# Optimization experiments

Hardware: AMD Instinct MI355X
Metric: run time of the kernel (lower is better)

Reference implementation:

```python
import jax, jax.numpy as jnp
import numpy as np

CAPACITY_FACTOR = 1.25


def setup_inputs() -> dict:
    key = jax.random.key(0)
    k1, k2, k3, k4 = jax.random.split(key, 4)
    B, T, H = 2, 2048, 1024
    E, F = 8, 2048
    x = jax.random.normal(k1, (B, T, H), dtype=jnp.float32)
    Wr = jax.random.normal(k2, (H, E), dtype=jnp.float32) * 0.02
    W1 = jax.random.normal(k3, (E, H, 2 * F), dtype=jnp.float32) * 0.02
    W2 = jax.random.normal(k4, (E, F, H), dtype=jnp.float32) * 0.02
    return {"x": x, "Wr": Wr, "W1": W1, "W2": W2}


def _moe_forward(x, Wr, W1, W2):
    B, T, H = x.shape
    E = Wr.shape[1]
    N = B * T
    cap = max(1, int(CAPACITY_FACTOR * (N * 2 / E)))  # static (shape-derived)

    flat_x = x.reshape(N, H)
    logits = flat_x @ Wr                      # [N, E] (train=False: no noise)
    gate = jax.nn.softmax(logits, axis=-1)
    top2_val, top2_idx = jax.lax.top_k(gate, 2)   # [N,2]

    # --- capacity bookkeeping, matching the torch sequential fill order ---
    e0, e1 = top2_idx[:, 0], top2_idx[:, 1]
    oh0 = jax.nn.one_hot(e0, E, dtype=jnp.int32)  # [N,E]
    oh1 = jax.nn.one_hot(e1, E, dtype=jnp.int32)
    # rank of each token within its expert's k=0 queue (flattened token order)
    pos0 = jnp.take_along_axis(jnp.cumsum(oh0, axis=0), top2_idx[:, :1], axis=1)[:, 0] - 1
    count0 = oh0.sum(axis=0)                      # tokens routed top-1 per expert
    used0 = jnp.minimum(count0, cap)              # slots consumed in k=0 pass
    keep0 = pos0 < cap
    # k=1 pass starts after the slots used by k=0
    pos1 = jnp.take_along_axis(jnp.cumsum(oh1, axis=0), top2_idx[:, 1:2], axis=1)[:, 0] - 1
    pos1 = pos1 + used0[e1]
    keep1 = pos1 < cap

    dummy = E * cap  # drop slot
    slot0 = jnp.where(keep0, e0 * cap + pos0, dummy)
    slot1 = jnp.where(keep1, e1 * cap + pos1, dummy)

    # --- dispatch: [E*cap+1, H] buffer (last row is the drop slot) ---
    buf = jnp.zeros((E * cap + 1, H), dtype=x.dtype)
    buf = buf.at[slot0].set(flat_x).at[slot1].set(flat_x)
    xe = buf[: E * cap].reshape(E, cap, H)

    # --- grouped expert FFN (SwiGLU) ---
    h = jnp.einsum("ech,ehf->ecf", xe, W1)        # [E, cap, 2F]
    a, b = jnp.split(h, 2, axis=-1)
    act = jax.nn.silu(a) * b                      # [E, cap, F]
    out = jnp.einsum("ecf,efh->ech", act, W2)     # [E, cap, H]
    out_flat = out.reshape(E * cap, H)

    # --- combine: gather back per token, weighted by gate values ---
    g0 = out_flat[jnp.where(keep0, slot0, 0)] * keep0[:, None]
    g1 = out_flat[jnp.where(keep1, slot1, 0)] * keep1[:, None]
    y = g0 * top2_val[:, 0:1] + g1 * top2_val[:, 1:2]
    y = y.reshape(B, T, H)

    # --- balance loss ---
    me = 1e-9
    prob_per_expert = gate.mean(axis=0)                 # == mean over (B,T)
    used1 = (oh1 * keep1[:, None].astype(jnp.int32)).sum(axis=0)
    used = (used0 + used1).astype(gate.dtype)
    frac_used = jnp.maximum(used, me) / (N * 2 + me)
    balance_loss = (prob_per_expert * frac_used).sum() * E
    return y, balance_loss


def reference(x, Wr, W1, W2):
    return _moe_forward(x, Wr, W1, W2)
```

## Files before the change

### kernel.cpp

```cpp
#include <hip/hip_runtime.h>
#include <cstdint>

#define E_    8
#define H_    1024
#define F_    2048
#define NTOK  4096
#define CAP   1280
#define ECAP  (E_*CAP)

typedef unsigned short u16;
typedef __attribute__((ext_vector_type(8))) short bf16x8;
typedef __attribute__((ext_vector_type(4))) float f32x4;
typedef __attribute__((ext_vector_type(4))) unsigned short u16x4;

__device__ __forceinline__ u16 f2bf(float f) {
  union { float f; uint32_t u; } v; v.f = f;
  uint32_t r = v.u + 0x7fffu + ((v.u >> 16) & 1u);
  return (u16)(r >> 16);
}

__device__ __forceinline__ void gld16(const void* gsrc, void* ldst) {
  auto g = reinterpret_cast<const __attribute__((address_space(1))) uint32_t*>(
      reinterpret_cast<uintptr_t>(gsrc));
  auto l = reinterpret_cast<__attribute__((address_space(3))) uint32_t*>(
      reinterpret_cast<uintptr_t>(ldst));
  __builtin_amdgcn_global_load_lds(g, l, 16, 0, 0);
}

__device__ __forceinline__ int swz(int row, int chunk) {
  return row * 64 + ((chunk ^ (row & 7)) * 8);
}

__global__ __launch_bounds__(256) void transpose_cvt_all(const float* __restrict__ W1,
                                                         const float* __restrict__ W2,
                                                         u16* __restrict__ W1T,
                                                         u16* __restrict__ W2T) {
  __shared__ float tile[64][65];
  int b = blockIdx.x;
  const float* in; u16* outp; int R, C, rt, ct;
  if (b < 8192) {
    int slab = b >> 10, t = b & 1023;
    rt = t >> 6; ct = t & 63;
    R = H_; C = 2 * F_;
    in = W1 + (size_t)slab * R * C;
    outp = W1T + (size_t)slab * R * C;
  } else {
    b -= 8192;
    int slab = b >> 9, t = b & 511;
    rt = t >> 4; ct = t & 15;
    R = F_; C = H_;
    in = W2 + (size_t)slab * R * C;
    outp = W2T + (size_t)slab * R * C;
  }
  int r0 = rt * 64, c0 = ct * 64;
  int tx = threadIdx.x, ty = threadIdx.y;
#pragma unroll
  for (int i = 0; i < 4; i++) {
    int row = ty + 16 * i;
    float4 v = *(const float4*)(in + (size_t)(r0 + row) * C + c0 + tx * 4);
    tile[row][tx * 4 + 0] = v.x;
    tile[row][tx * 4 + 1] = v.y;
    tile[row][tx * 4 + 2] = v.z;
    tile[row][tx * 4 + 3] = v.w;
  }
  __syncthreads();
#pragma unroll
  for (int i = 0; i < 4; i++) {
    int c = ty + 16 * i;
    u16x4 bq;
    bq.x = f2bf(tile[tx * 4 + 0][c]);
    bq.y = f2bf(tile[tx * 4 + 1][c]);
    bq.z = f2bf(tile[tx * 4 + 2][c]);
    bq.w = f2bf(tile[tx * 4 + 3][c]);
    *(u16x4*)(outp + (size_t)(c0 + c) * R + r0 + tx * 4) = bq;
  }
}

__global__ __launch_bounds__(256) void router_kernel(const float* __restrict__ x,
                                                     const float* __restrict__ Wr,
                                                     int* __restrict__ e0o, int* __restrict__ e1o,
                                                     float* __restrict__ v0o, float* __restrict__ v1o,
                                                     float* __restrict__ partial) {
  int w = threadIdx.x >> 6, l = threadIdx.x & 63;
  int t = blockIdx.x * 4 + w;
  const float* xr = x + (size_t)t * H_;
  float acc[8] = {0.f,0.f,0.f,0.f,0.f,0.f,0.f,0.f};
#pragma unroll
  for (int it = 0; it < 16; ++it) {
    int h = it * 64 + l;
    float xv = xr[h];
    const float4* wr = (const float4*)(Wr + h * 8);
    float4 wa = wr[0], wb = wr[1];
    acc[0] += xv * wa.x; acc[1] += xv * wa.y; acc[2] += xv * wa.z; acc[3] += xv * wa.w;
    acc[4] += xv * wb.x; acc[5] += xv * wb.y; acc[6] += xv * wb.z; acc[7] += xv * wb.w;
  }
#pragma unroll
  for (int e = 0; e < 8; ++e)
#pragma unroll
    for (int off = 32; off; off >>= 1)
      acc[e] += __shfl_xor(acc[e], off);

  __shared__ float pg[4][8];
  if (l == 0) {
    float mx = acc[0];
#pragma unroll
    for (int e = 1; e < 8; ++e) mx = fmaxf(mx, acc[e]);
    float g[8], s = 0.f;
#pragma unroll
    for (int e = 0; e < 8; ++e) { g[e] = __expf(acc[e] - mx); s += g[e]; }
    float inv = 1.f / s;
#pragma unroll
    for (int e = 0; e < 8; ++e) g[e] *= inv;
    int b0 = 0; float m0 = g[0];
#pragma unroll
    for (int e = 1; e < 8; ++e) if (g[e] > m0) { m0 = g[e]; b0 = e; }
    int b1 = -1; float m1 = -1.f;
#pragma unroll
    for (int e = 0; e < 8; ++e) if (e != b0 && g[e] > m1) { m1 = g[e]; b1 = e; }
    e0o[t] = b0; e1o[t] = b1; v0o[t] = m0; v1o[t] = m1;
#pragma unroll
    for (int e = 0; e < 8; ++e) pg[w][e] = g[e];
  }
  __syncthreads();
  if (threadIdx.x < 8) {
    int e = threadIdx.x;
    partial[blockIdx.x * 8 + e] = pg[0][e] + pg[1][e] + pg[2][e] + pg[3][e];
  }
}

__global__ __launch_bounds__(256) void scan_kernel(const int* __restrict__ e0i, const int* __restrict__ e1i,
                                                   const float* __restrict__ partial,
                                                   int* __restrict__ slot0, int* __restrict__ slot1,
                                                   int* __restrict__ used_out,
                                                   float* __restrict__ bl_out) {
  __shared__ int c0[256][8], c1[256][8];
  __shared__ float gs[256][8];
  __shared__ int used0_s[8], tot1_s[8];
  int tid = threadIdx.x;

  int le0[16], le1[16];
  int lc0[8] = {0,0,0,0,0,0,0,0}, lc1[8] = {0,0,0,0,0,0,0,0};
  for (int i = 0; i < 16; ++i) {
    int t = tid * 16 + i;
    le0[i] = e0i[t]; le1[i] = e1i[t];
    lc0[le0[i]]++; lc1[le1[i]]++;
  }
#pragma unroll
  for (int e = 0; e < 8; ++e) { c0[tid][e] = lc0[e]; c1[tid][e] = lc1[e]; }

  float g[8] = {0.f,0.f,0.f,0.f,0.f,0.f,0.f,0.f};
  for (int rr = 0; rr < 4; ++rr)
#pragma unroll
    for (int e = 0; e < 8; ++e) g[e] += partial[(tid + rr * 256) * 8 + e];
#pragma unroll
  for (int e = 0; e < 8; ++e) gs[tid][e] = g[e];
  __syncthreads();

  for (int d = 1; d < 256; d <<= 1) {
    int t0[8], t1[8];
    bool a = (tid >= d);
    if (a) {
#pragma unroll
      for (int e = 0; e < 8; ++e) { t0[e] = c0[tid - d][e]; t1[e] = c1[tid - d][e]; }
    }
    __syncthreads();
    if (a) {
#pragma unroll
      for (int e = 0; e < 8; ++e) { c0[tid][e] += t0[e]; c1[tid][e] += t1[e]; }
    }
    __syncthreads();
  }
  for (int s = 128; s > 0; s >>= 1) {
    if (tid < s)
#pragma unroll
      for (int e = 0; e < 8; ++e) gs[tid][e] += gs[tid + s][e];
    __syncthreads();
  }
  if (tid < 8) {
    int e = tid;
    int u0 = min(c0[255][e], CAP);
    int t1 = c1[255][e];
    used0_s[e] = u0;
    tot1_s[e] = t1;
    used_out[e] = u0 + min(t1, max(0, CAP - u0));
  }
  __syncthreads();

  int ex0[8], ex1[8];
#pragma unroll
  for (int e = 0; e < 8; ++e) { ex0[e] = c0[tid][e] - lc0[e]; ex1[e] = c1[tid][e] - lc1[e]; }
  int r0c[8] = {0,0,0,0,0,0,0,0}, r1c[8] = {0,0,0,0,0,0,0,0};
  for (int i = 0; i < 16; ++i) {
    int t = tid * 16 + i;
    int e = le0[i];
    int pos = ex0[e] + r0c[e]; r0c[e]++;
    slot0[t] = (pos < CAP) ? (e * CAP + pos) : -1;
    e = le1[i];
    pos = ex1[e] + r1c[e] + used0_s[e]; r1c[e]++;
    slot1[t] = (pos < CAP) ? (e * CAP + pos) : -1;
  }

  if (tid == 0) {
    float bl = 0.f;
    for (int e = 0; e < 8; ++e) {
      int u1 = min(tot1_s[e], max(0, CAP - used0_s[e]));
      float used = (float)(used0_s[e] + u1);
      float fu = fmaxf(used, 1e-9f) / (8192.f + 1e-9f);
      bl += (gs[0][e] / (float)NTOK) * fu;
    }
    bl_out[0] = bl * 8.f;
  }
}

__global__ __launch_bounds__(256) void scatter_kernel(const float* __restrict__ x,
                                                      const int* __restrict__ slot0,
                                                      const int* __restrict__ slot1,
                                                      u16* __restrict__ xe) {
  int t = blockIdx.x, tid = threadIdx.x;
  float4 vv = *(const float4*)(x + (size_t)t * H_ + tid * 4);
  u16x4 b;
  b.x = f2bf(vv.x); b.y = f2bf(vv.y); b.z = f2bf(vv.z); b.w = f2bf(vv.w);
  int s0 = slot0[t], s1 = slot1[t];
  if (s0 >= 0) *(u16x4*)(xe + (size_t)s0 * H_ + tid * 4) = b;
  if (s1 >= 0) *(u16x4*)(xe + (size_t)s1 * H_ + tid * 4) = b;
}

__global__ __launch_bounds__(256, 2) void gemm1_kernel(const u16* __restrict__ xe,
                                                       const u16* __restrict__ W1T,
                                                       const int* __restrict__ used_tot,
                                                       u16* __restrict__ act) {
  const int mbase = blockIdx.y * 128;
  const int e = mbase / 1280;
  if (mbase - e * 1280 >= used_tot[e]) return;

  __shared__ u16 As[128 * 64];
  __shared__ u16 Bsa[64 * 64];
  __shared__ u16 Bsb[64 * 64];
  const int tid = threadIdx.x;
  const int w = tid >> 6, l = tid & 63;
  const int wm = w & 1, wn = w >> 1;
  const int nbase = blockIdx.x * 64;
  const u16* Ap = xe + (size_t)mbase * H_;
  const u16* Ba = W1T + (size_t)e * 4096 * H_ + (size_t)nbase * H_;
  const u16* Bb = Ba + (size_t)F_ * H_;
  const int lrow = l >> 3;
  const int lcol = (((l & 7) ^ lrow) * 8);

  f32x4 acca[4][2] = {};
  f32x4 accb[4][2] = {};

  for (int kt = 0; kt < 16; ++kt) {
    int k0 = kt * 64;
#pragma unroll
    for (int r = 0; r < 4; ++r) {
      int row0 = w * 32 + r * 8;
      gld16(Ap + (size_t)(row0 + lrow) * H_ + k0 + lcol, &As[row0 * 64]);
    }
#pragma unroll
    for (int r = 0; r < 2; ++r) {
      int row0 = w * 16 + r * 8;
      gld16(Ba + (size_t)(row0 + lrow) * H_ + k0 + lcol, &Bsa[row0 * 64]);
      gld16(Bb + (size_t)(row0 + lrow) * H_ + k0 + lcol, &Bsb[row0 * 64]);
    }
    __syncthreads();
#pragma unroll
    for (int kk = 0; kk < 64; kk += 32) {
      const int ck = (kk >> 3) + (l >> 4);
      bf16x8 af[4], ba[2], bb[2];
#pragma unroll
      for (int i = 0; i < 4; ++i)
        af[i] = *(const bf16x8*)&As[swz(wm * 64 + i * 16 + (l & 15), ck)];
#pragma unroll
      for (int j = 0; j < 2; ++j) {
        ba[j] = *(const bf16x8*)&Bsa[swz(wn * 32 + j * 16 + (l & 15), ck)];
        bb[j] = *(const bf16x8*)&Bsb[swz(wn * 32 + j * 16 + (l & 15), ck)];
      }
#pragma unroll
      for (int i = 0; i < 4; ++i)
#pragma unroll
        for (int j = 0; j < 2; ++j) {
          acca[i][j] = __builtin_amdgcn_mfma_f32_16x16x32_bf16(af[i], ba[j], acca[i][j], 0, 0, 0);
          accb[i][j] = __builtin_amdgcn_mfma_f32_16x16x32_bf16(af[i], bb[j], accb[i][j], 0, 0, 0);
        }
    }
    __syncthreads();
  }
#pragma unroll
  for (int i = 0; i < 4; ++i)
#pragma unroll
    for (int j = 0; j < 2; ++j)
#pragma unroll
      for (int r = 0; r < 4; ++r) {
        int m = mbase + wm * 64 + i * 16 + (l >> 4) * 4 + r;
        int f = nbase + wn * 32 + j * 16 + (l & 15);
        float a = acca[i][j][r];
        float b = accb[i][j][r];
        float s = a / (1.f + __expf(-a));
        act[(size_t)m * F_ + f] = f2bf(s * b);
      }
}

__global__ __launch_bounds__(256, 2) void gemm2_kernel(const u16* __restrict__ act,
                                                       const u16* __restrict__ W2T,
                                                       const int* __restrict__ used_tot,
                                                       float* __restrict__ outb) {
  const int mbase = blockIdx.y * 128;
  const int e = mbase / 1280;
  if (mbase - e * 1280 >= used_tot[e]) return;

  __shared__ u16 As[128 * 64];
  __shared__ u16 Bs[128 * 64];
  const int tid = threadIdx.x;
  const int w = tid >> 6, l = tid & 63;
  const int wm = w & 1, wn = w >> 1;
  const int nbase = blockIdx.x * 128;
  const u16* Ap = act + (size_t)mbase * F_;
  const u16* Bp = W2T + (size_t)e * H_ * F_ + (size_t)nbase * F_;
  const int lrow = l >> 3;
  const int lcol = (((l & 7) ^ lrow) * 8);

  f32x4 acc[4][4] = {};

  for (int kt = 0; kt < 32; ++kt) {
    int k0 = kt * 64;
#pragma unroll
    for (int r = 0; r < 4; ++r) {
      int row0 = w * 32 + r * 8;
      gld16(Ap + (size_t)(row0 + lrow) * F_ + k0 + lcol, &As[row0 * 64]);
      gld16(Bp + (size_t)(row0 + lrow) * F_ + k0 + lcol, &Bs[row0 * 64]);
    }
    __syncthreads();
#pragma unroll
    for (int kk = 0; kk < 64; kk += 32) {
      const int ck = (kk >> 3) + (l >> 4);
      bf16x8 af[4], bf[4];
#pragma unroll
      for (int i = 0; i < 4; ++i)
        af[i] = *(const bf16x8*)&As[swz(wm * 64 + i * 16 + (l & 15), ck)];
#pragma unroll
      for (int j = 0; j < 4; ++j)
        bf[j] = *(const bf16x8*)&Bs[swz(wn * 64 + j * 16 + (l & 15), ck)];
#pragma unroll
      for (int i = 0; i < 4; ++i)
#pragma unroll
        for (int j = 0; j < 4; ++j)
          acc[i][j] = __builtin_amdgcn_mfma_f32_16x16x32_bf16(af[i], bf[j], acc[i][j], 0, 0, 0);
    }
    __syncthreads();
  }
#pragma unroll
  for (int i = 0; i < 4; ++i)
#pragma unroll
    for (int j = 0; j < 4; ++j)
#pragma unroll
      for (int r = 0; r < 4; ++r) {
        int m = mbase + wm * 64 + i * 16 + (l >> 4) * 4 + r;
        int n = nbase + wn * 64 + j * 16 + (l & 15);
        outb[(size_t)m * H_ + n] = acc[i][j][r];
      }
}

__global__ __launch_bounds__(256) void combine_kernel(const float* __restrict__ outb,
                                                      const int* __restrict__ slot0,
                                                      const int* __restrict__ slot1,
                                                      const float* __restrict__ v0,
                                                      const float* __restrict__ v1,
                                                      float* __restrict__ y) {
  int t = blockIdx.x, tid = threadIdx.x;
  int s0 = slot0[t], s1 = slot1[t];
  float w0 = v0[t], w1 = v1[t];
  float4 r; r.x = 0.f; r.y = 0.f; r.z = 0.f; r.w = 0.f;
  if (s0 >= 0) {
    float4 a = *(const float4*)(outb + (size_t)s0 * H_ + tid * 4);
    r.x += w0 * a.x; r.y += w0 * a.y; r.z += w0 * a.z; r.w += w0 * a.w;
  }
  if (s1 >= 0) {
    float4 a = *(const float4*)(outb + (size_t)s1 * H_ + tid * 4);
    r.x += w1 * a.x; r.y += w1 * a.y; r.z += w1 * a.z; r.w += w1 * a.w;
  }
  *(float4*)(y + (size_t)t * H_ + tid * 4) = r;
}

#define OFF_W1T   ((size_t)0)
#define OFF_W2T   ((size_t)67108864)
#define OFF_XE    ((size_t)100663296)
#define OFF_ACT   ((size_t)121634816)
#define OFF_OUTB  ((size_t)163577856)
#define OFF_SLOT0 ((size_t)205520896)
#define OFF_SLOT1 ((size_t)205537280)
#define OFF_V0    ((size_t)205553664)
#define OFF_V1    ((size_t)205570048)
#define OFF_E0    ((size_t)205586432)
#define OFF_E1    ((size_t)205602816)
#define OFF_PART  ((size_t)205619200)
#define OFF_USED  ((size_t)205651968)

extern "C" void kernel_launch(void* const* d_in, const int* in_sizes, int n_in,
                              void* d_out, int out_size, void* d_ws, size_t ws_size,
                              hipStream_t stream) {
  const float* x  = (const float*)d_in[0];
  const float* Wr = (const float*)d_in[1];
  const float* W1 = (const float*)d_in[2];
  const float* W2 = (const float*)d_in[3];
  float* out = (float*)d_out;

  uint8_t* ws = (uint8_t*)d_ws;
  u16*   W1T   = (u16*)(ws + OFF_W1T);
  u16*   W2T   = (u16*)(ws + OFF_W2T);
  u16*   xe    = (u16*)(ws + OFF_XE);
  u16*   act   = (u16*)(ws + OFF_ACT);
  float* outb  = (float*)(ws + OFF_OUTB);
  int*   slot0 = (int*)(ws + OFF_SLOT0);
  int*   slot1 = (int*)(ws + OFF_SLOT1);
  float* v0    = (float*)(ws + OFF_V0);
  float* v1    = (float*)(ws + OFF_V1);
  int*   e0    = (int*)(ws + OFF_E0);
  int*   e1    = (int*)(ws + OFF_E1);
  float* part  = (float*)(ws + OFF_PART);
  int*   used  = (int*)(ws + OFF_USED);

  transpose_cvt_all<<<12288, dim3(16, 16), 0, stream>>>(W1, W2, W1T, W2T);

  router_kernel<<<NTOK / 4, 256, 0, stream>>>(x, Wr, e0, e1, v0, v1, part);
  scan_kernel<<<1, 256, 0, stream>>>(e0, e1, part, slot0, slot1, used, out + (size_t)NTOK * H_);
  scatter_kernel<<<NTOK, 256, 0, stream>>>(x, slot0, slot1, xe);

  gemm1_kernel<<<dim3(F_ / 64, ECAP / 128), 256, 0, stream>>>(xe, W1T, used, act);
  gemm2_kernel<<<dim3(H_ / 128, ECAP / 128), 256, 0, stream>>>(act, W2T, used, outb);

  combine_kernel<<<NTOK, 256, 0, stream>>>(outb, slot0, slot1, v0, v1, out);
}
```

Before: 224.6 us.

## Fuse router into weight transpose kernel and convert to bf16 before LDS staging

Merges the weight transpose/convert kernel and the router kernel into one launch, with extra blocks handling routing so it overlaps the transpose work and saves a launch. The transpose now converts fp32 to bf16 before staging in shared memory, which halves the LDS footprint, and writes 16-byte vectors of 8 bf16 values instead of 8-byte ones. Column reads from the padded u16 tile may introduce bank conflicts.

```diff
diff --git a/kernel.cpp b/kernel.cpp
--- a/kernel.cpp
+++ b/kernel.cpp
@@ -12,6 +12,7 @@
 typedef __attribute__((ext_vector_type(8))) short bf16x8;
 typedef __attribute__((ext_vector_type(4))) float f32x4;
 typedef __attribute__((ext_vector_type(4))) unsigned short u16x4;
+typedef __attribute__((ext_vector_type(8))) unsigned short u16x8;
 
 __device__ __forceinline__ u16 f2bf(float f) {
   union { float f; uint32_t u; } v; v.f = f;
@@ -31,100 +32,101 @@
   return row * 64 + ((chunk ^ (row & 7)) * 8);
 }
 
-__global__ __launch_bounds__(256) void transpose_cvt_all(const float* __restrict__ W1,
-                                                         const float* __restrict__ W2,
-                                                         u16* __restrict__ W1T,
-                                                         u16* __restrict__ W2T) {
-  __shared__ float tile[64][65];
+__global__ __launch_bounds__(256) void prep_kernel(const float* __restrict__ W1,
+                                                   const float* __restrict__ W2,
+                                                   u16* __restrict__ W1T,
+                                                   u16* __restrict__ W2T,
+                                                   const float* __restrict__ x,
+                                                   const float* __restrict__ Wr,
+                                                   int* __restrict__ e0o, int* __restrict__ e1o,
+                                                   float* __restrict__ v0o, float* __restrict__ v1o,
+                                                   float* __restrict__ partial) {
   int b = blockIdx.x;
-  const float* in; u16* outp; int R, C, rt, ct;
-  if (b < 8192) {
-    int slab = b >> 10, t = b & 1023;
-    rt = t >> 6; ct = t & 63;
-    R = H_; C = 2 * F_;
-    in = W1 + (size_t)slab * R * C;
-    outp = W1T + (size_t)slab * R * C;
+  if (b < 12288) {
+    __shared__ u16 tile[64 * 70];
+    const float* in; u16* outp; int R, C, rt, ct;
+    if (b < 8192) {
+      int slab = b >> 10, t = b & 1023;
+      rt = t >> 6; ct = t & 63;
+      R = H_; C = 2 * F_;
+      in = W1 + (size_t)slab * R * C;
+      outp = W1T + (size_t)slab * R * C;
+    } else {
+      int bb = b - 8192;
+      int slab = bb >> 9, t = bb & 511;
+      rt = t >> 4; ct = t & 15;
+      R = F_; C = H_;
+      in = W2 + (size_t)slab * R * C;
+      outp = W2T + (size_t)slab * R * C;
+    }
+    int r0 = rt * 64, c0 = ct * 64;
+    int t = threadIdx.x;
+    int col4 = t & 15, row = t >> 4;
+#pragma unroll
+    for (int i = 0; i < 4; i++) {
+      int r = row + 16 * i;
+      float4 v = *(const float4*)(in + (size_t)(r0 + r) * C + c0 + col4 * 4);
+      u16x4 q;
+      q.x = f2bf(v.x); q.y = f2bf(v.y); q.z = f2bf(v.z); q.w = f2bf(v.w);
+      *(u16x4*)&tile[r * 70 + col4 * 4] = q;
+    }
+    __syncthreads();
+    int lane8 = t & 7, cc = t >> 3;
+#pragma unroll
+    for (int j = 0; j < 2; j++) {
+      int c = cc + 32 * j;
+      u16x8 q;
+#pragma unroll
+      for (int k = 0; k < 8; k++) q[k] = tile[(lane8 * 8 + k) * 70 + c];
+      *(u16x8*)(outp + (size_t)(c0 + c) * R + r0 + lane8 * 8) = q;
+    }
   } else {
-    b -= 8192;
-    int slab = b >> 9, t = b & 511;
-    rt = t >> 4; ct = t & 15;
-    R = F_; C = H_;
-    in = W2 + (size_t)slab * R * C;
-    outp = W2T + (size_t)slab * R * C;
-  }
-  int r0 = rt * 64, c0 = ct * 64;
-  int tx = threadIdx.x, ty = threadIdx.y;
-#pragma unroll
-  for (int i = 0; i < 4; i++) {
-    int row = ty + 16 * i;
-    float4 v = *(const float4*)(in + (size_t)(r0 + row) * C + c0 + tx * 4);
-    tile[row][tx * 4 + 0] = v.x;
-    tile[row][tx * 4 + 1] = v.y;
-    tile[row][tx * 4 + 2] = v.z;
-    tile[row][tx * 4 + 3] = v.w;
-  }
-  __syncthreads();
-#pragma unroll
-  for (int i = 0; i < 4; i++) {
-    int c = ty + 16 * i;
-    u16x4 bq;
-    bq.x = f2bf(tile[tx * 4 + 0][c]);
-    bq.y = f2bf(tile[tx * 4 + 1][c]);
-    bq.z = f2bf(tile[tx * 4 + 2][c]);
-    bq.w = f2bf(tile[tx * 4 + 3][c]);
-    *(u16x4*)(outp + (size_t)(c0 + c) * R + r0 + tx * 4) = bq;
-  }
-}
-
-__global__ __launch_bounds__(256) void router_kernel(const float* __restrict__ x,
-                                                     const float* __restrict__ Wr,
-                                                     int* __restrict__ e0o, int* __restrict__ e1o,
-                                                     float* __restrict__ v0o, float* __restrict__ v1o,
-                                                     float* __restrict__ partial) {
-  int w = threadIdx.x >> 6, l = threadIdx.x & 63;
-  int t = blockIdx.x * 4 + w;
-  const float* xr = x + (size_t)t * H_;
-  float acc[8] = {0.f,0.f,0.f,0.f,0.f,0.f,0.f,0.f};
-#pragma unroll
-  for (int it = 0; it < 16; ++it) {
-    int h = it * 64 + l;
-    float xv = xr[h];
-    const float4* wr = (const float4*)(Wr + h * 8);
-    float4 wa = wr[0], wb = wr[1];
-    acc[0] += xv * wa.x; acc[1] += xv * wa.y; acc[2] += xv * wa.z; acc[3] += xv * wa.w;
-    acc[4] += xv * wb.x; acc[5] += xv * wb.y; acc[6] += xv * wb.z; acc[7] += xv * wb.w;
-  }
-#pragma unroll
-  for (int e = 0; e < 8; ++e)
-#pragma unroll
-    for (int off = 32; off; off >>= 1)
-      acc[e] += __shfl_xor(acc[e], off);
-
-  __shared__ float pg[4][8];
-  if (l == 0) {
-    float mx = acc[0];
-#pragma unroll
-    for (int e = 1; e < 8; ++e) mx = fmaxf(mx, acc[e]);
-    float g[8], s = 0.f;
-#pragma unroll
-    for (int e = 0; e < 8; ++e) { g[e] = __expf(acc[e] - mx); s += g[e]; }
-    float inv = 1.f / s;
-#pragma unroll
-    for (int e = 0; e < 8; ++e) g[e] *= inv;
-    int b0 = 0; float m0 = g[0];
-#pragma unroll
-    for (int e = 1; e < 8; ++e) if (g[e] > m0) { m0 = g[e]; b0 = e; }
-    int b1 = -1; float m1 = -1.f;
-#pragma unroll
-    for (int e = 0; e < 8; ++e) if (e != b0 && g[e] > m1) { m1 = g[e]; b1 = e; }
-    e0o[t] = b0; e1o[t] = b1; v0o[t] = m0; v1o[t] = m1;
-#pragma unroll
-    for (int e = 0; e < 8; ++e) pg[w][e] = g[e];
-  }
-  __syncthreads();
-  if (threadIdx.x < 8) {
-    int e = threadIdx.x;
-    partial[blockIdx.x * 8 + e] = pg[0][e] + pg[1][e] + pg[2][e] + pg[3][e];
+    int blk = b - 12288;
+    int w = threadIdx.x >> 6, l = threadIdx.x & 63;
+    int t = blk * 4 + w;
+    const float* xr = x + (size_t)t * H_;
+    float acc[8] = {0.f,0.f,0.f,0.f,0.f,0.f,0.f,0.f};
+#pragma unroll
+    for (int it = 0; it < 16; ++it) {
+      int h = it * 64 + l;
+      float xv = xr[h];
+      const float4* wr = (const float4*)(Wr + h * 8);
+      float4 wa = wr[0], wb = wr[1];
+      acc[0] += xv * wa.x; acc[1] += xv * wa.y; acc[2] += xv * wa.z; acc[3] += xv * wa.w;
+      acc[4] += xv * wb.x; acc[5] += xv * wb.y; acc[6] += xv * wb.z; acc[7] += xv * wb.w;
+    }
+#pragma unroll
+    for (int e = 0; e < 8; ++e)
+#pragma unroll
+      for (int off = 32; off; off >>= 1)
+        acc[e] += __shfl_xor(acc[e], off);
+
+    __shared__ float pg[4][8];
+    if (l == 0) {
+      float mx = acc[0];
+#pragma unroll
+      for (int e = 1; e < 8; ++e) mx = fmaxf(mx, acc[e]);
+      float g[8], s = 0.f;
+#pragma unroll
+      for (int e = 0; e < 8; ++e) { g[e] = __expf(acc[e] - mx); s += g[e]; }
+      float inv = 1.f / s;
+#pragma unroll
+      for (int e = 0; e < 8; ++e) g[e] *= inv;
+      int b0 = 0; float m0 = g[0];
+#pragma unroll
+      for (int e = 1; e < 8; ++e) if (g[e] > m0) { m0 = g[e]; b0 = e; }
+      int b1 = -1; float m1 = -1.f;
+#pragma unroll
+      for (int e = 0; e < 8; ++e) if (e != b0 && g[e] > m1) { m1 = g[e]; b1 = e; }
+      e0o[t] = b0; e1o[t] = b1; v0o[t] = m0; v1o[t] = m1;
+#pragma unroll
+      for (int e = 0; e < 8; ++e) pg[w][e] = g[e];
+    }
+    __syncthreads();
+    if (threadIdx.x < 8) {
+      int e = threadIdx.x;
+      partial[blk * 8 + e] = pg[0][e] + pg[1][e] + pg[2][e] + pg[3][e];
+    }
   }
 }
 
@@ -419,9 +421,8 @@
   float* part  = (float*)(ws + OFF_PART);
   int*   used  = (int*)(ws + OFF_USED);
 
-  transpose_cvt_all<<<12288, dim3(16, 16), 0, stream>>>(W1, W2, W1T, W2T);
-
-  router_kernel<<<NTOK / 4, 256, 0, stream>>>(x, Wr, e0, e1, v0, v1, part);
+  prep_kernel<<<13312, 256, 0, stream>>>(W1, W2, W1T, W2T, x, Wr, e0, e1, v0, v1, part);
+
   scan_kernel<<<1, 256, 0, stream>>>(e0, e1, part, slot0, slot1, used, out + (size_t)NTOK * H_);
   scatter_kernel<<<NTOK, 256, 0, stream>>>(x, slot0, slot1, xe);
 
```

New measurement: 222.4 us. No clear change (-1.0%).
